# Performance work log

Measured on AMD Instinct MI355X. Metric: run time of the kernel, lower is better.

The kernel has to match this reference:

```python
import jax, jax.numpy as jnp
import numpy as np

FS = 4            # filter_size
DIV_FLOW = 20.0   # PWCNet flow scale
T = 0.5           # timestep


def _upsample4(flow, H, W):
    # nn.Upsample(scale_factor=4, mode='bilinear', align_corners=False)
    B, C = flow.shape[0], flow.shape[1]
    return jax.image.resize(flow, (B, C, H, W), method='bilinear')


def _flow_project(flow):
    """DAIN FlowProjection: forward-scatter -flow to the 4 integer neighbors of
    (x+fx, y+fy), average by hit count, fill holes with valid 4-neighbor mean."""
    B, _, H, W = flow.shape
    gx = jnp.arange(W, dtype=flow.dtype)[None, None, :]
    gy = jnp.arange(H, dtype=flow.dtype)[None, :, None]
    x2 = gx + flow[:, 0]
    y2 = gy + flow[:, 1]
    valid = (x2 >= 0) & (x2 <= W - 1) & (y2 >= 0) & (y2 <= H - 1)
    xf = jnp.floor(x2).astype(jnp.int32)
    yf = jnp.floor(y2).astype(jnp.int32)
    vfx = jnp.where(valid, -flow[:, 0], 0.0).reshape(-1)
    vfy = jnp.where(valid, -flow[:, 1], 0.0).reshape(-1)
    vc = valid.astype(flow.dtype).reshape(-1)
    boff = (jnp.arange(B, dtype=jnp.int32) * (H * W))[:, None, None]
    accx = jnp.zeros(B * H * W, flow.dtype)
    accy = jnp.zeros(B * H * W, flow.dtype)
    cnt = jnp.zeros(B * H * W, flow.dtype)
    for dy in (0, 1):
        for dx in (0, 1):
            xi = jnp.clip(xf + dx, 0, W - 1)
            yi = jnp.clip(yf + dy, 0, H - 1)
            idx = (boff + yi * W + xi).reshape(-1)
            accx = accx.at[idx].add(vfx)
            accy = accy.at[idx].add(vfy)
            cnt = cnt.at[idx].add(vc)
    cnt = cnt.reshape(B, H, W)
    avg = jnp.stack([accx.reshape(B, H, W), accy.reshape(B, H, W)], axis=1)
    avg = avg / jnp.maximum(cnt, 1.0)[:, None]
    hole = cnt <= 0                       # (B,H,W)
    ok = (~hole).astype(flow.dtype)[:, None]
    fp = jnp.pad(avg * ok, ((0, 0), (0, 0), (1, 1), (1, 1)))
    op = jnp.pad(ok, ((0, 0), (0, 0), (1, 1), (1, 1)))
    num = fp[:, :, :-2, 1:-1] + fp[:, :, 2:, 1:-1] + fp[:, :, 1:-1, :-2] + fp[:, :, 1:-1, 2:]
    den = op[:, :, :-2, 1:-1] + op[:, :, 2:, 1:-1] + op[:, :, 1:-1, :-2] + op[:, :, 1:-1, 2:]
    filled = num / jnp.maximum(den, 1.0)
    return jnp.where(hole[:, None], filled, avg)


def _filter_interp(img, flow, filt, fs):
    """DAIN FilterInterpolation: out(p) = sum_{j,i} filt[j*fs+i,p] *
    bilinear(img, p + flow + (i+1-fs/2, j+1-fs/2))."""
    B, C, H, W = img.shape
    gx = jnp.arange(W, dtype=img.dtype)[None, None, :]
    gy = jnp.arange(H, dtype=img.dtype)[None, :, None]
    x2 = jnp.clip(gx + flow[:, 0], 0.0, W - 1.0)
    y2 = jnp.clip(gy + flow[:, 1], 0.0, H - 1.0)
    xf = jnp.floor(x2).astype(jnp.int32)
    yf = jnp.floor(y2).astype(jnp.int32)
    a = (x2 - xf)[:, None]   # (B,1,H,W)
    b = (y2 - yf)[:, None]
    w00 = (1.0 - a) * (1.0 - b)
    w10 = a * (1.0 - b)
    w01 = (1.0 - a) * b
    w11 = a * b
    flat = img.reshape(B, C, H * W)

    def gather(yi, xi):
        idx = (yi * W + xi).reshape(B, 1, H * W)
        return jnp.take_along_axis(flat, idx, axis=2).reshape(B, C, H, W)

    off = 1 - fs // 2
    out = jnp.zeros_like(img)
    for j in range(fs):
        yT = jnp.clip(yf + j + off, 0, H - 1)
        yB = jnp.clip(yf + j + off + 1, 0, H - 1)
        for i in range(fs):
            xL = jnp.clip(xf + i + off, 0, W - 1)
            xR = jnp.clip(xf + i + off + 1, 0, W - 1)
            v = (w00 * gather(yT, xL) + w10 * gather(yT, xR)
                 + w01 * gather(yB, xL) + w11 * gather(yB, xR))
            out = out + v * filt[:, j * fs + i][:, None]
    return out


def setup_inputs() -> dict:
    key = jax.random.key(0)
    k = jax.random.split(key, 6)
    B, H, W = 4, 384, 512
    return {
        'input0': jax.random.uniform(k[0], (B, 3, H, W), jnp.float32),
        'input2': jax.random.uniform(k[1], (B, 3, H, W), jnp.float32),
        'flow01': jax.random.normal(k[2], (B, 2, H // 4, W // 4), jnp.float32),
        'flow10': jax.random.normal(k[3], (B, 2, H // 4, W // 4), jnp.float32),
        'filt0': jax.random.uniform(k[4], (B, FS * FS, H, W), jnp.float32),
        'filt1': jax.random.uniform(k[5], (B, FS * FS, H, W), jnp.float32),
    }


def reference(input0, input2, flow01, flow10, filt0, filt1):
    B, _, H, W = input0.shape
    scale = DIV_FLOW * T
    f01 = _upsample4(flow01 * scale, H, W)   # F_{0->2} scaled to t=0.5
    f10 = _upsample4(flow10 * scale, H, W)   # F_{2->0} scaled to t=0.5
    Ft0 = _flow_project(f01)                 # F_{t->0}
    Ft2 = _flow_project(f10)                 # F_{t->2}
    ref0 = _filter_interp(input0, Ft0, filt0, FS)
    ref2 = _filter_interp(input2, Ft2, filt1, FS)
    return 0.5 * (ref0 + ref2)
```

## Files before the change

kernel.cpp:

```cpp
#include <hip/hip_runtime.h>

#define HH 384
#define WW 512
#define NB 4
#define HWP (HH * WW)
#define NPIX (NB * HWP)
#define SH 96
#define SW 128
#define SHW (SH * SW)

#define MBOUND 40
#define BAND 4
#define NBANDS (HH / BAND)
#define OV_CAP 65536

static __device__ __forceinline__ float upsample_flow_f32(const float* __restrict__ f, int y, int x) {
    float sx = __fadd_rn(__fmul_rn((float)x, 0.25f), -0.375f);
    float sy = __fadd_rn(__fmul_rn((float)y, 0.25f), -0.375f);
    float fx0 = floorf(sx), fy0 = floorf(sy);
    float wx = __fsub_rn(sx, fx0);
    float wy = __fsub_rn(sy, fy0);
    int ix = (int)fx0, iy = (int)fy0;
    int x0 = max(ix, 0), x1 = min(ix + 1, SW - 1);
    int y0 = max(iy, 0), y1 = min(iy + 1, SH - 1);
    float v00 = __fmul_rn(10.0f, f[y0 * SW + x0]);
    float v01 = __fmul_rn(10.0f, f[y0 * SW + x1]);
    float v10 = __fmul_rn(10.0f, f[y1 * SW + x0]);
    float v11 = __fmul_rn(10.0f, f[y1 * SW + x1]);
    float omx = __fsub_rn(1.0f, wx);
    float omy = __fsub_rn(1.0f, wy);
    float w00 = __fmul_rn(omx, omy);
    float w10 = __fmul_rn(wx, omy);
    float w01 = __fmul_rn(omx, wy);
    float w11 = __fmul_rn(wx, wy);
    float s = __fmul_rn(w00, v00);
    s = __fadd_rn(s, __fmul_rn(w10, v01));
    s = __fadd_rn(s, __fmul_rn(w01, v10));
    s = __fadd_rn(s, __fmul_rn(w11, v11));
    return s;
}

__global__ __launch_bounds__(256) void upsample_k(const float* __restrict__ flow01,
                                                  const float* __restrict__ flow10,
                                                  float* __restrict__ Fu, float* __restrict__ ovf) {
    int idx = blockIdx.x * blockDim.x + threadIdx.x;
    if (idx >= NPIX) return;
    int side = blockIdx.y;
    const float* flow = side ? flow10 : flow01;
    int x = idx % WW;
    int y = (idx / WW) % HH;
    int b = idx / HWP;
    const float* fp = flow + b * 2 * SHW;
    float fx = upsample_flow_f32(fp, y, x);
    float fy = upsample_flow_f32(fp + SHW, y, x);
    float* F = Fu + side * 2 * NPIX;
    F[idx] = fx;
    F[NPIX + idx] = fy;
    float x2 = __fadd_rn((float)x, fx);
    float y2 = __fadd_rn((float)y, fy);
    bool valid = (x2 >= 0.0f && x2 <= (float)(WW - 1) && y2 >= 0.0f && y2 <= (float)(HH - 1));
    bool banded = (fy >= -(float)MBOUND && fy < (float)MBOUND);
    if (valid && !banded) {
        int xf = (int)floorf(x2);
        int yf = (int)floorf(y2);
        int key = side * NPIX + b * HWP + yf * WW + xf;
        int slot = atomicAdd((int*)ovf, 1);
        if (slot >= 0 && slot < OV_CAP) {
            ((int*)ovf)[64 + slot] = key;
            ovf[64 + OV_CAP + slot] = -fx;
            ovf[64 + 2 * OV_CAP + slot] = -fy;
        }
    }
}

__global__ __launch_bounds__(256) void row_gather_k(const float* __restrict__ Fu,
                                                    const float* __restrict__ ovf,
                                                    float* __restrict__ g0, float* __restrict__ g1) {
    __shared__ float acc[3][BAND][WW];
    int bid = blockIdx.x;
    int slab = bid & 7;
    int side = slab >> 2;
    int b = slab & 3;
    int t0 = (bid >> 3) * BAND;

    const float* Fx = Fu + side * 2 * NPIX + b * HWP;
    const float* Fyp = Fx + NPIX;

    float* A = &acc[0][0][0];
    for (int k = threadIdx.x; k < 3 * BAND * WW; k += 256) A[k] = 0.0f;
    __syncthreads();

    int sLo = max(t0 - MBOUND, 0);
    int sHi = min(t0 + BAND - 1 + MBOUND, HH - 1);
    for (int s = sLo; s <= sHi; ++s) {
        int rowoff = s * WW + 2 * threadIdx.x;
        float2 fxv = *(const float2*)(Fx + rowoff);
        float2 fyv = *(const float2*)(Fyp + rowoff);
        float sf = (float)s;
        #pragma unroll
        for (int u = 0; u < 2; ++u) {
            int xx = 2 * threadIdx.x + u;
            float fx = u ? fxv.y : fxv.x;
            float fy = u ? fyv.y : fyv.x;
            float x2 = __fadd_rn((float)xx, fx);
            float y2 = __fadd_rn(sf, fy);
            if (x2 >= 0.0f && x2 <= (float)(WW - 1) && y2 >= 0.0f && y2 <= (float)(HH - 1)
                && fy >= -(float)MBOUND && fy < (float)MBOUND) {
                int yf = (int)floorf(y2);
                int r = yf - t0;
                if (r >= 0 && r < BAND) {
                    int xf = (int)floorf(x2);
                    atomicAdd(&acc[0][r][xf], -fx);
                    atomicAdd(&acc[1][r][xf], -fy);
                    atomicAdd(&acc[2][r][xf], 1.0f);
                }
            }
        }
    }

    int n = ((const int*)ovf)[0];
    n = (n < 0) ? 0 : ((n > OV_CAP) ? OV_CAP : n);
    int lo = t0 * WW, hi = (t0 + BAND) * WW;
    int keybase = side * NPIX + b * HWP;
    for (int i = threadIdx.x; i < n; i += 256) {
        int rel = ((const int*)ovf)[64 + i] - keybase;
        if (rel >= lo && rel < hi) {
            int r = rel / WW - t0;
            int xf = rel % WW;
            atomicAdd(&acc[0][r][xf], ovf[64 + OV_CAP + i]);
            atomicAdd(&acc[1][r][xf], ovf[64 + 2 * OV_CAP + i]);
            atomicAdd(&acc[2][r][xf], 1.0f);
        }
    }
    __syncthreads();

    float* G = (side ? g1 : g0) + b * HWP;
    for (int k = threadIdx.x; k < 3 * BAND * WW; k += 256) {
        int plane = k / (BAND * WW);
        int rem = k % (BAND * WW);
        G[plane * NPIX + t0 * WW + rem] = A[k];
    }
}

static __device__ __forceinline__ void box_sum(const float* __restrict__ G, int b, int y, int x,
                                               float& ax, float& ay, float& c) {
    const float* Gx = G;
    const float* Gy = G + NPIX;
    const float* Gc = G + 2 * NPIX;
    float wxs1 = (x == WW - 1) ? 2.0f : 1.0f;
    float wys1 = (y == HH - 1) ? 2.0f : 1.0f;
    float sx = 0.0f, sy = 0.0f, sc = 0.0f;
    int base = b * HWP;
    #pragma unroll
    for (int j = 0; j < 2; j++) {
        int ey = y - 1 + j;
        if (ey < 0) continue;
        float wy = j ? wys1 : 1.0f;
        #pragma unroll
        for (int i = 0; i < 2; i++) {
            int ex = x - 1 + i;
            if (ex < 0) continue;
            float w = wy * ((i ? wxs1 : 1.0f));
            int o = base + ey * WW + ex;
            sx += w * Gx[o];
            sy += w * Gy[o];
            sc += w * Gc[o];
        }
    }
    ax = sx; ay = sy; c = sc;
}

__global__ __launch_bounds__(256) void fill2_k(const float* __restrict__ g0, const float* __restrict__ g1,
                                               float* __restrict__ Ft0, float* __restrict__ Ft2) {
    int idx = blockIdx.x * blockDim.x + threadIdx.x;
    if (idx >= NPIX) return;
    int side = blockIdx.y;
    const float* G = side ? g1 : g0;
    float* Ft = side ? Ft2 : Ft0;
    int x = idx % WW;
    int y = (idx / WW) % HH;
    int b = idx / HWP;
    float ax, ay, c;
    box_sum(G, b, y, x, ax, ay, c);
    float ox, oy;
    if (c > 0.0f) {
        ox = ax / c;
        oy = ay / c;
    } else {
        float nx = 0.0f, ny = 0.0f, den = 0.0f;
        float bx, by, bc;
        if (y > 0)      { box_sum(G, b, y - 1, x, bx, by, bc); if (bc > 0.0f) { nx += bx / bc; ny += by / bc; den += 1.0f; } }
        if (y < HH - 1) { box_sum(G, b, y + 1, x, bx, by, bc); if (bc > 0.0f) { nx += bx / bc; ny += by / bc; den += 1.0f; } }
        if (x > 0)      { box_sum(G, b, y, x - 1, bx, by, bc); if (bc > 0.0f) { nx += bx / bc; ny += by / bc; den += 1.0f; } }
        if (x < WW - 1) { box_sum(G, b, y, x + 1, bx, by, bc); if (bc > 0.0f) { nx += bx / bc; ny += by / bc; den += 1.0f; } }
        float inv = 1.0f / fmaxf(den, 1.0f);
        ox = nx * inv;
        oy = ny * inv;
    }
    Ft[idx] = ox;
    Ft[NPIX + idx] = oy;
}

__global__ void interp_k(const float* __restrict__ img0, const float* __restrict__ img2,
                         const float* __restrict__ filt0, const float* __restrict__ filt1,
                         const float* __restrict__ Ft0, const float* __restrict__ Ft2,
                         float* __restrict__ out) {
    int x = blockIdx.x * 64 + threadIdx.x;
    int y = blockIdx.y * 4 + threadIdx.y;
    int bz = blockIdx.z;
    int side = bz >> 2;
    int b = bz & 3;
    const float* img  = side ? img2  : img0;
    const float* filt = side ? filt1 : filt0;
    const float* Ft   = side ? Ft2   : Ft0;

    int idx = b * HWP + y * WW + x;
    float fx = Ft[idx];
    float fy = Ft[NPIX + idx];
    float x2 = fminf(fmaxf((float)x + fx, 0.0f), (float)(WW - 1));
    float y2 = fminf(fmaxf((float)y + fy, 0.0f), (float)(HH - 1));
    float xff = floorf(x2), yff = floorf(y2);
    int xf = (int)xff, yf = (int)yff;
    float a  = x2 - xff;
    float bb = y2 - yff;
    float w00 = (1.0f - a) * (1.0f - bb);
    float w10 = a * (1.0f - bb);
    float w01 = (1.0f - a) * bb;
    float w11 = a * bb;

    float F[4][4];
    #pragma unroll
    for (int k = 0; k < 16; k++) {
        F[k >> 2][k & 3] = filt[((b * 16 + k) * HH + y) * WW + x];
    }
    float Cf[5][5];
    #pragma unroll
    for (int r = 0; r < 5; r++) {
        #pragma unroll
        for (int sc = 0; sc < 5; sc++) {
            float v = 0.0f;
            if (r < 4 && sc < 4)   v += w00 * F[r][sc];
            if (r < 4 && sc >= 1)  v += w10 * F[r][sc - 1];
            if (r >= 1 && sc < 4)  v += w01 * F[r - 1][sc];
            if (r >= 1 && sc >= 1) v += w11 * F[r - 1][sc - 1];
            Cf[r][sc] = v;
        }
    }
    int rows[5];
    #pragma unroll
    for (int r = 0; r < 5; r++) rows[r] = min(max(yf - 1 + r, 0), HH - 1);

    bool interior = (xf >= 1) && (xf <= WW - 4);
    if (interior) {
        int x0 = xf - 1;
        #pragma unroll
        for (int c = 0; c < 3; c++) {
            const float* ip = img + (b * 3 + c) * HWP;
            float accv = 0.0f;
            #pragma unroll
            for (int r = 0; r < 5; r++) {
                const float* rp = ip + rows[r] * WW + x0;
                float wrow[5];
                __builtin_memcpy(wrow, rp, 5 * sizeof(float));
                #pragma unroll
                for (int sc = 0; sc < 5; sc++) {
                    accv += Cf[r][sc] * wrow[sc];
                }
            }
            unsafeAtomicAdd(&out[((b * 3 + c) * HH + y) * WW + x], 0.5f * accv);
        }
    } else {
        int cols[5];
        #pragma unroll
        for (int sc = 0; sc < 5; sc++) cols[sc] = min(max(xf - 1 + sc, 0), WW - 1);
        #pragma unroll
        for (int c = 0; c < 3; c++) {
            const float* ip = img + (b * 3 + c) * HWP;
            float accv = 0.0f;
            #pragma unroll
            for (int r = 0; r < 5; r++) {
                const float* rp = ip + rows[r] * WW;
                #pragma unroll
                for (int sc = 0; sc < 5; sc++) {
                    accv += Cf[r][sc] * rp[cols[sc]];
                }
            }
            unsafeAtomicAdd(&out[((b * 3 + c) * HH + y) * WW + x], 0.5f * accv);
        }
    }
}

extern "C" void kernel_launch(void* const* d_in, const int* in_sizes, int n_in,
                              void* d_out, int out_size, void* d_ws, size_t ws_size,
                              hipStream_t stream) {
    const float* input0 = (const float*)d_in[0];
    const float* input2 = (const float*)d_in[1];
    const float* flow01 = (const float*)d_in[2];
    const float* flow10 = (const float*)d_in[3];
    const float* filt0  = (const float*)d_in[4];
    const float* filt1  = (const float*)d_in[5];
    float* out = (float*)d_out;

    float* ws = (float*)d_ws;
    float* g0   = ws;
    float* g1   = ws + 3 * NPIX;
    float* Fu   = ws + 6 * NPIX;
    float* Ft0  = ws + 6 * NPIX;
    float* Ft2  = ws + 8 * NPIX;
    float* ovf  = out;

    const int BS = 256;
    const int NBLK = (NPIX + BS - 1) / BS;

    hipMemsetAsync(ovf, 0, 256, stream);

    upsample_k<<<dim3(NBLK, 2), BS, 0, stream>>>(flow01, flow10, Fu, ovf);
    row_gather_k<<<dim3(2 * NB * NBANDS), BS, 0, stream>>>(Fu, ovf, g0, g1);
    hipMemsetAsync(out, 0, (size_t)3 * NPIX * sizeof(float), stream);
    fill2_k<<<dim3(NBLK, 2), BS, 0, stream>>>(g0, g1, Ft0, Ft2);
    interp_k<<<dim3(WW / 64, HH / 4, NB * 2), dim3(64, 4), 0, stream>>>(
        input0, input2, filt0, filt1, Ft0, Ft2, out);
}
```

Measured before the change: 272.7 us.

## Fuse hole-filling into interpolation and combine both sides in one kernel

The separate fill kernel that wrote projected flow to global memory is folded into the interpolation kernel, so the projected flow is computed in registers from the gathered accumulators. Each thread now handles both sides for its pixel and writes the averaged output directly. This removes the output memset and the atomic adds, along with one kernel launch and the Ft write/read round trip. The cost is higher register pressure and half as many blocks in the grid, and the box-sum recompute now sits inside the heavier kernel.

```diff
diff --git a/kernel.cpp b/kernel.cpp
--- a/kernel.cpp
+++ b/kernel.cpp
@@ -170,22 +170,16 @@
     ax = sx; ay = sy; c = sc;
 }
 
-__global__ __launch_bounds__(256) void fill2_k(const float* __restrict__ g0, const float* __restrict__ g1,
-                                               float* __restrict__ Ft0, float* __restrict__ Ft2) {
-    int idx = blockIdx.x * blockDim.x + threadIdx.x;
-    if (idx >= NPIX) return;
-    int side = blockIdx.y;
-    const float* G = side ? g1 : g0;
-    float* Ft = side ? Ft2 : Ft0;
-    int x = idx % WW;
-    int y = (idx / WW) % HH;
-    int b = idx / HWP;
+static __device__ __forceinline__ void side_interp(const float* __restrict__ G,
+                                                   const float* __restrict__ img,
+                                                   const float* __restrict__ filt,
+                                                   int b, int x, int y, float res[3]) {
     float ax, ay, c;
     box_sum(G, b, y, x, ax, ay, c);
-    float ox, oy;
+    float fx, fy;
     if (c > 0.0f) {
-        ox = ax / c;
-        oy = ay / c;
+        fx = ax / c;
+        fy = ay / c;
     } else {
         float nx = 0.0f, ny = 0.0f, den = 0.0f;
         float bx, by, bc;
@@ -194,29 +188,10 @@
         if (x > 0)      { box_sum(G, b, y, x - 1, bx, by, bc); if (bc > 0.0f) { nx += bx / bc; ny += by / bc; den += 1.0f; } }
         if (x < WW - 1) { box_sum(G, b, y, x + 1, bx, by, bc); if (bc > 0.0f) { nx += bx / bc; ny += by / bc; den += 1.0f; } }
         float inv = 1.0f / fmaxf(den, 1.0f);
-        ox = nx * inv;
-        oy = ny * inv;
-    }
-    Ft[idx] = ox;
-    Ft[NPIX + idx] = oy;
-}
-
-__global__ void interp_k(const float* __restrict__ img0, const float* __restrict__ img2,
-                         const float* __restrict__ filt0, const float* __restrict__ filt1,
-                         const float* __restrict__ Ft0, const float* __restrict__ Ft2,
-                         float* __restrict__ out) {
-    int x = blockIdx.x * 64 + threadIdx.x;
-    int y = blockIdx.y * 4 + threadIdx.y;
-    int bz = blockIdx.z;
-    int side = bz >> 2;
-    int b = bz & 3;
-    const float* img  = side ? img2  : img0;
-    const float* filt = side ? filt1 : filt0;
-    const float* Ft   = side ? Ft2   : Ft0;
-
-    int idx = b * HWP + y * WW + x;
-    float fx = Ft[idx];
-    float fy = Ft[NPIX + idx];
+        fx = nx * inv;
+        fy = ny * inv;
+    }
+
     float x2 = fminf(fmaxf((float)x + fx, 0.0f), (float)(WW - 1));
     float y2 = fminf(fmaxf((float)y + fy, 0.0f), (float)(HH - 1));
     float xff = floorf(x2), yff = floorf(y2);
@@ -254,8 +229,8 @@
     if (interior) {
         int x0 = xf - 1;
         #pragma unroll
-        for (int c = 0; c < 3; c++) {
-            const float* ip = img + (b * 3 + c) * HWP;
+        for (int ch = 0; ch < 3; ch++) {
+            const float* ip = img + (b * 3 + ch) * HWP;
             float accv = 0.0f;
             #pragma unroll
             for (int r = 0; r < 5; r++) {
@@ -267,15 +242,15 @@
                     accv += Cf[r][sc] * wrow[sc];
                 }
             }
-            unsafeAtomicAdd(&out[((b * 3 + c) * HH + y) * WW + x], 0.5f * accv);
+            res[ch] = accv;
         }
     } else {
         int cols[5];
         #pragma unroll
         for (int sc = 0; sc < 5; sc++) cols[sc] = min(max(xf - 1 + sc, 0), WW - 1);
         #pragma unroll
-        for (int c = 0; c < 3; c++) {
-            const float* ip = img + (b * 3 + c) * HWP;
+        for (int ch = 0; ch < 3; ch++) {
+            const float* ip = img + (b * 3 + ch) * HWP;
             float accv = 0.0f;
             #pragma unroll
             for (int r = 0; r < 5; r++) {
@@ -285,8 +260,30 @@
                     accv += Cf[r][sc] * rp[cols[sc]];
                 }
             }
-            unsafeAtomicAdd(&out[((b * 3 + c) * HH + y) * WW + x], 0.5f * accv);
-        }
+            res[ch] = accv;
+        }
+    }
+}
+
+__global__ __launch_bounds__(256) void interp2_k(const float* __restrict__ img0,
+                                                 const float* __restrict__ img2,
+                                                 const float* __restrict__ filt0,
+                                                 const float* __restrict__ filt1,
+                                                 const float* __restrict__ g0,
+                                                 const float* __restrict__ g1,
+                                                 float* __restrict__ out) {
+    int x = blockIdx.x * 64 + threadIdx.x;
+    int y = blockIdx.y * 4 + threadIdx.y;
+    int b = blockIdx.z;
+
+    float r0[3], r1[3];
+    side_interp(g0, img0, filt0, b, x, y, r0);
+    side_interp(g1, img2, filt1, b, x, y, r1);
+
+    #pragma unroll
+    for (int ch = 0; ch < 3; ch++) {
+        out[((b * 3 + ch) * HH + y) * WW + x] =
+            __fadd_rn(__fmul_rn(0.5f, r0[ch]), __fmul_rn(0.5f, r1[ch]));
     }
 }
 
@@ -305,8 +302,6 @@
     float* g0   = ws;
     float* g1   = ws + 3 * NPIX;
     float* Fu   = ws + 6 * NPIX;
-    float* Ft0  = ws + 6 * NPIX;
-    float* Ft2  = ws + 8 * NPIX;
     float* ovf  = out;
 
     const int BS = 256;
@@ -316,8 +311,6 @@
 
     upsample_k<<<dim3(NBLK, 2), BS, 0, stream>>>(flow01, flow10, Fu, ovf);
     row_gather_k<<<dim3(2 * NB * NBANDS), BS, 0, stream>>>(Fu, ovf, g0, g1);
-    hipMemsetAsync(out, 0, (size_t)3 * NPIX * sizeof(float), stream);
-    fill2_k<<<dim3(NBLK, 2), BS, 0, stream>>>(g0, g1, Ft0, Ft2);
-    interp_k<<<dim3(WW / 64, HH / 4, NB * 2), dim3(64, 4), 0, stream>>>(
-        input0, input2, filt0, filt1, Ft0, Ft2, out);
-}
+    interp2_k<<<dim3(WW / 64, HH / 4, NB), dim3(64, 4), 0, stream>>>(
+        input0, input2, filt0, filt1, g0, g1, out);
+}
```

After: 283.2 us. 1.04x slower.

## Fuse projection fill into row-gather kernel using halo rows in LDS

Applied to the files above, without the earlier changes.

Merges the hole-fill pass into the row-gather kernel. Each band now accumulates BAND+3 rows (a halo) in shared memory so the box sums and neighbour fill can be computed from LDS, and the result is written straight to Ft0/Ft2. This removes the g0/g1 global accumulation buffers, their write-out and re-read, and one kernel launch. In exchange each block scans more source rows, holds a larger LDS footprint (about 43 KB), and recomputes the halo rows that neighbouring bands also accumulate.

```diff
diff --git a/kernel.cpp b/kernel.cpp
--- a/kernel.cpp
+++ b/kernel.cpp
@@ -12,6 +12,7 @@
 #define MBOUND 40
 #define BAND 4
 #define NBANDS (HH / BAND)
+#define NROWS (BAND + 3)
 #define OV_CAP 65536
 
 static __device__ __forceinline__ float upsample_flow_f32(const float* __restrict__ f, int y, int x) {
@@ -73,25 +74,51 @@
     }
 }
 
-__global__ __launch_bounds__(256) void row_gather_k(const float* __restrict__ Fu,
-                                                    const float* __restrict__ ovf,
-                                                    float* __restrict__ g0, float* __restrict__ g1) {
-    __shared__ float acc[3][BAND][WW];
+static __device__ __forceinline__ void box_sum_lds(const float (&acc)[3][NROWS][WW], int rbase,
+                                                   int y, int x, float& ax, float& ay, float& c) {
+    float wxs1 = (x == WW - 1) ? 2.0f : 1.0f;
+    float wys1 = (y == HH - 1) ? 2.0f : 1.0f;
+    float sx = 0.0f, sy = 0.0f, sc = 0.0f;
+    #pragma unroll
+    for (int j = 0; j < 2; j++) {
+        int ey = y - 1 + j;
+        if (ey < 0) continue;
+        float wy = j ? wys1 : 1.0f;
+        int rr = ey - rbase;
+        #pragma unroll
+        for (int i = 0; i < 2; i++) {
+            int ex = x - 1 + i;
+            if (ex < 0) continue;
+            float w = wy * ((i ? wxs1 : 1.0f));
+            sx += w * acc[0][rr][ex];
+            sy += w * acc[1][rr][ex];
+            sc += w * acc[2][rr][ex];
+        }
+    }
+    ax = sx; ay = sy; c = sc;
+}
+
+__global__ __launch_bounds__(256) void row_gather_fill_k(const float* __restrict__ Fu,
+                                                         const float* __restrict__ ovf,
+                                                         float* __restrict__ Ft0,
+                                                         float* __restrict__ Ft2) {
+    __shared__ float acc[3][NROWS][WW];
     int bid = blockIdx.x;
     int slab = bid & 7;
     int side = slab >> 2;
     int b = slab & 3;
     int t0 = (bid >> 3) * BAND;
+    int rbase = t0 - 2;
 
     const float* Fx = Fu + side * 2 * NPIX + b * HWP;
     const float* Fyp = Fx + NPIX;
 
     float* A = &acc[0][0][0];
-    for (int k = threadIdx.x; k < 3 * BAND * WW; k += 256) A[k] = 0.0f;
+    for (int k = threadIdx.x; k < 3 * NROWS * WW; k += 256) A[k] = 0.0f;
     __syncthreads();
 
-    int sLo = max(t0 - MBOUND, 0);
-    int sHi = min(t0 + BAND - 1 + MBOUND, HH - 1);
+    int sLo = max(t0 - 2 - (MBOUND - 1), 0);
+    int sHi = min(t0 + BAND + MBOUND, HH - 1);
     for (int s = sLo; s <= sHi; ++s) {
         int rowoff = s * WW + 2 * threadIdx.x;
         float2 fxv = *(const float2*)(Fx + rowoff);
@@ -107,8 +134,8 @@
             if (x2 >= 0.0f && x2 <= (float)(WW - 1) && y2 >= 0.0f && y2 <= (float)(HH - 1)
                 && fy >= -(float)MBOUND && fy < (float)MBOUND) {
                 int yf = (int)floorf(y2);
-                int r = yf - t0;
-                if (r >= 0 && r < BAND) {
+                int r = yf - rbase;
+                if (r >= 0 && r < NROWS) {
                     int xf = (int)floorf(x2);
                     atomicAdd(&acc[0][r][xf], -fx);
                     atomicAdd(&acc[1][r][xf], -fy);
@@ -120,12 +147,13 @@
 
     int n = ((const int*)ovf)[0];
     n = (n < 0) ? 0 : ((n > OV_CAP) ? OV_CAP : n);
-    int lo = t0 * WW, hi = (t0 + BAND) * WW;
+    int lo = max(rbase, 0) * WW;
+    int hi = (min(t0 + BAND, HH - 1) + 1) * WW;
     int keybase = side * NPIX + b * HWP;
     for (int i = threadIdx.x; i < n; i += 256) {
         int rel = ((const int*)ovf)[64 + i] - keybase;
         if (rel >= lo && rel < hi) {
-            int r = rel / WW - t0;
+            int r = rel / WW - rbase;
             int xf = rel % WW;
             atomicAdd(&acc[0][r][xf], ovf[64 + OV_CAP + i]);
             atomicAdd(&acc[1][r][xf], ovf[64 + 2 * OV_CAP + i]);
@@ -134,71 +162,31 @@
     }
     __syncthreads();
 
-    float* G = (side ? g1 : g0) + b * HWP;
-    for (int k = threadIdx.x; k < 3 * BAND * WW; k += 256) {
-        int plane = k / (BAND * WW);
-        int rem = k % (BAND * WW);
-        G[plane * NPIX + t0 * WW + rem] = A[k];
-    }
-}
-
-static __device__ __forceinline__ void box_sum(const float* __restrict__ G, int b, int y, int x,
-                                               float& ax, float& ay, float& c) {
-    const float* Gx = G;
-    const float* Gy = G + NPIX;
-    const float* Gc = G + 2 * NPIX;
-    float wxs1 = (x == WW - 1) ? 2.0f : 1.0f;
-    float wys1 = (y == HH - 1) ? 2.0f : 1.0f;
-    float sx = 0.0f, sy = 0.0f, sc = 0.0f;
-    int base = b * HWP;
-    #pragma unroll
-    for (int j = 0; j < 2; j++) {
-        int ey = y - 1 + j;
-        if (ey < 0) continue;
-        float wy = j ? wys1 : 1.0f;
-        #pragma unroll
-        for (int i = 0; i < 2; i++) {
-            int ex = x - 1 + i;
-            if (ex < 0) continue;
-            float w = wy * ((i ? wxs1 : 1.0f));
-            int o = base + ey * WW + ex;
-            sx += w * Gx[o];
-            sy += w * Gy[o];
-            sc += w * Gc[o];
-        }
-    }
-    ax = sx; ay = sy; c = sc;
-}
-
-__global__ __launch_bounds__(256) void fill2_k(const float* __restrict__ g0, const float* __restrict__ g1,
-                                               float* __restrict__ Ft0, float* __restrict__ Ft2) {
-    int idx = blockIdx.x * blockDim.x + threadIdx.x;
-    if (idx >= NPIX) return;
-    int side = blockIdx.y;
-    const float* G = side ? g1 : g0;
     float* Ft = side ? Ft2 : Ft0;
-    int x = idx % WW;
-    int y = (idx / WW) % HH;
-    int b = idx / HWP;
-    float ax, ay, c;
-    box_sum(G, b, y, x, ax, ay, c);
-    float ox, oy;
-    if (c > 0.0f) {
-        ox = ax / c;
-        oy = ay / c;
-    } else {
-        float nx = 0.0f, ny = 0.0f, den = 0.0f;
-        float bx, by, bc;
-        if (y > 0)      { box_sum(G, b, y - 1, x, bx, by, bc); if (bc > 0.0f) { nx += bx / bc; ny += by / bc; den += 1.0f; } }
-        if (y < HH - 1) { box_sum(G, b, y + 1, x, bx, by, bc); if (bc > 0.0f) { nx += bx / bc; ny += by / bc; den += 1.0f; } }
-        if (x > 0)      { box_sum(G, b, y, x - 1, bx, by, bc); if (bc > 0.0f) { nx += bx / bc; ny += by / bc; den += 1.0f; } }
-        if (x < WW - 1) { box_sum(G, b, y, x + 1, bx, by, bc); if (bc > 0.0f) { nx += bx / bc; ny += by / bc; den += 1.0f; } }
-        float inv = 1.0f / fmaxf(den, 1.0f);
-        ox = nx * inv;
-        oy = ny * inv;
-    }
-    Ft[idx] = ox;
-    Ft[NPIX + idx] = oy;
+    for (int k = threadIdx.x; k < BAND * WW; k += 256) {
+        int y = t0 + k / WW;
+        int x = k % WW;
+        float ax, ay, c;
+        box_sum_lds(acc, rbase, y, x, ax, ay, c);
+        float fx, fy;
+        if (c > 0.0f) {
+            fx = ax / c;
+            fy = ay / c;
+        } else {
+            float nx = 0.0f, ny = 0.0f, den = 0.0f;
+            float bx, by, bc;
+            if (y > 0)      { box_sum_lds(acc, rbase, y - 1, x, bx, by, bc); if (bc > 0.0f) { nx += bx / bc; ny += by / bc; den += 1.0f; } }
+            if (y < HH - 1) { box_sum_lds(acc, rbase, y + 1, x, bx, by, bc); if (bc > 0.0f) { nx += bx / bc; ny += by / bc; den += 1.0f; } }
+            if (x > 0)      { box_sum_lds(acc, rbase, y, x - 1, bx, by, bc); if (bc > 0.0f) { nx += bx / bc; ny += by / bc; den += 1.0f; } }
+            if (x < WW - 1) { box_sum_lds(acc, rbase, y, x + 1, bx, by, bc); if (bc > 0.0f) { nx += bx / bc; ny += by / bc; den += 1.0f; } }
+            float inv = 1.0f / fmaxf(den, 1.0f);
+            fx = nx * inv;
+            fy = ny * inv;
+        }
+        int o = b * HWP + y * WW + x;
+        Ft[o] = fx;
+        Ft[NPIX + o] = fy;
+    }
 }
 
 __global__ void interp_k(const float* __restrict__ img0, const float* __restrict__ img2,
@@ -302,11 +290,9 @@
     float* out = (float*)d_out;
 
     float* ws = (float*)d_ws;
-    float* g0   = ws;
-    float* g1   = ws + 3 * NPIX;
-    float* Fu   = ws + 6 * NPIX;
-    float* Ft0  = ws + 6 * NPIX;
-    float* Ft2  = ws + 8 * NPIX;
+    float* Fu   = ws;
+    float* Ft0  = ws + 4 * NPIX;
+    float* Ft2  = ws + 6 * NPIX;
     float* ovf  = out;
 
     const int BS = 256;
@@ -315,9 +301,8 @@
     hipMemsetAsync(ovf, 0, 256, stream);
 
     upsample_k<<<dim3(NBLK, 2), BS, 0, stream>>>(flow01, flow10, Fu, ovf);
-    row_gather_k<<<dim3(2 * NB * NBANDS), BS, 0, stream>>>(Fu, ovf, g0, g1);
+    row_gather_fill_k<<<dim3(2 * NB * NBANDS), BS, 0, stream>>>(Fu, ovf, Ft0, Ft2);
     hipMemsetAsync(out, 0, (size_t)3 * NPIX * sizeof(float), stream);
-    fill2_k<<<dim3(NBLK, 2), BS, 0, stream>>>(g0, g1, Ft0, Ft2);
     interp_k<<<dim3(WW / 64, HH / 4, NB * 2), dim3(64, 4), 0, stream>>>(
         input0, input2, filt0, filt1, Ft0, Ft2, out);
 }
```

Result: no change. 277.4 us (+1.7%).
